# Kernel tuning notes

Hardware: AMD Instinct MI355X
Metric: run time of the kernel (lower is better)

The kernel has to match this reference:

```python
import jax, jax.numpy as jnp
import numpy as np

B, L, S, H, E = 2, 2048, 2048, 16, 64
EPS = 1e-8


def setup_inputs() -> dict:
    key = jax.random.key(0)
    k1, k2, k3, k4, k5 = jax.random.split(key, 5)
    query = jax.random.normal(k1, (B, L, H, E), dtype=jnp.float32)
    key_t = jax.random.normal(k2, (B, S, H, E), dtype=jnp.float32)
    value = jax.random.normal(k3, (B, S, H, E), dtype=jnp.float32)
    mask_miss_k = jax.random.randint(k4, (B, S, 1), 0, 2).astype(bool)
    mask_miss_q = jax.random.randint(k5, (B, L, 1), 0, 2).astype(bool)
    # monotone per-batch positions -> standard causal structure
    pos = jnp.broadcast_to(jnp.arange(L, dtype=jnp.int32)[None, :, None], (B, L, 1))
    return {"query": query, "key": key_t, "value": value,
            "mask_miss_k": mask_miss_k, "mask_miss_q": mask_miss_q,
            "pos": pos, "causal_mask": 1}


def reference(query, key, value, mask_miss_k, mask_miss_q, pos, causal_mask):
    # query: (B,L,H,E); key/value: (B,S,H,E)
    E_ = query.shape[-1]
    scale = 1.0 / np.sqrt(E_)
    scores = jnp.einsum('blhe,bshe->bhls', query, key)  # (B,H,L,S)
    if causal_mask:
        p = pos[..., 0]  # (B,L)
        causal_add = jnp.where(p[:, None, :] > p[:, :, None],
                               -jnp.inf, 0.0).astype(scores.dtype)  # (B,L,S)
        scores = scores + causal_add[:, None, :, :]
    # additive -inf masks for missing keys / queries
    m_k = jnp.where(mask_miss_k[..., 0][:, None, None, :], -jnp.inf, 0.0).astype(scores.dtype)
    m_q = jnp.where(mask_miss_q[..., 0][:, None, :, None], -jnp.inf, 0.0).astype(scores.dtype)
    # NOTE: scale multiplies (scores + M_k) exactly as in the original
    att = jnp.maximum(jax.nn.softmax(scale * (scores + m_k), axis=-1) + m_q, 0.0)
    # entropy of (post-relu, possibly unnormalized) attention weights
    entropy = -jnp.sum(att * jnp.log(jnp.clip(att, EPS, None)), axis=-1)  # (B,H,L)
    entropy = jnp.nan_to_num(entropy, nan=0.0)
    A = jnp.nan_to_num(att)  # dropout p=0 -> identity, then nan_to_num
    V = jnp.einsum('bhls,bshd->blhd', A, value)  # (B,L,H,E)
    return V, A, entropy
```

## Files before the change

kernel.cpp:

```cpp
#include <hip/hip_runtime.h>

#define BB 2
#define LL 2048
#define SS 2048
#define HH 16
#define EE 64
#define HE (HH*EE)
#define BL 128
#define TS 64
#define NT2 32
#define SCALEF 0.125f
#define NEGBIG (-1e30f)

typedef __bf16 bf8 __attribute__((ext_vector_type(8)));
typedef float f4v __attribute__((ext_vector_type(4)));
typedef unsigned int u32;
typedef unsigned short u16;

#define V_ELEMS  ((size_t)BB*LL*HH*EE)
#define A_BASE   (V_ELEMS)
#define ENT_BASE (A_BASE + (size_t)BB*HH*LL*SS)

__device__ __forceinline__ u16 bfb(float f) {
    u32 u = __builtin_bit_cast(u32, f);
    return (u16)((u + 0x7fffu + ((u >> 16) & 1u)) >> 16);
}
__device__ __forceinline__ int swz8(int r) { return (((r) & 7) ^ (((r) >> 3) & 7)) << 4; }

__device__ __forceinline__ f4v mfma16(bf8 a, bf8 b, f4v c) {
    return __builtin_amdgcn_mfma_f32_16x16x32_bf16(a, b, c, 0, 0, 0);
}
__device__ __forceinline__ int maskv(const void* p, int i, int isB) {
    return isB ? (int)((const unsigned char*)p)[i] : ((const int*)p)[i];
}
__device__ __forceinline__ void barrier_lds() {
    asm volatile("s_waitcnt lgkmcnt(0)" ::: "memory");
    __builtin_amdgcn_s_barrier();
    asm volatile("" ::: "memory");
}
__device__ __forceinline__ uint4 pack8(float4 f0, float4 f1) {
    uint4 wv;
    wv.x = bfb(f0.x) | ((u32)bfb(f0.y) << 16);
    wv.y = bfb(f0.z) | ((u32)bfb(f0.w) << 16);
    wv.z = bfb(f1.x) | ((u32)bfb(f1.y) << 16);
    wv.w = bfb(f1.z) | ((u32)bfb(f1.w) << 16);
    return wv;
}

__device__ __forceinline__ void stage128x64(const float* __restrict__ src,
                                            char* lds, int tid) {
    const int r = tid >> 2, seg = tid & 3;
    const float* rp = src + (size_t)r * HE + seg * 16;
    float4 f0 = *(const float4*)(rp + 0);
    float4 f1 = *(const float4*)(rp + 4);
    float4 f2 = *(const float4*)(rp + 8);
    float4 f3 = *(const float4*)(rp + 12);
    const int base = r * 128 + seg * 32;
    *(uint4*)(void*)(lds + ((base +  0) ^ swz8(r))) = pack8(f0, f1);
    *(uint4*)(void*)(lds + ((base + 16) ^ swz8(r))) = pack8(f2, f3);
}

__global__ __launch_bounds__(512) void k_fused(
    const float* __restrict__ Qg, const float* __restrict__ Kg, const float* __restrict__ Vg,
    const void* __restrict__ mk, const void* __restrict__ mq,
    float* __restrict__ outF)
{
    __shared__ __align__(16) char ldsA[16384];
    __shared__ __align__(16) char ldsK[8192];
    __shared__ __align__(16) char ldsVT[8192];
    __shared__ float ldsKM[SS];
    __shared__ int sFlag;

    const int blk = blockIdx.x;
    const int bh  = (blk & 7) + (((blk >> 3) & 3) << 3);
    const int pair = blk >> 5;
    const int b = bh >> 4, h = bh & 15;
    const int tid = threadIdx.x;
    const int w = tid >> 6, lane = tid & 63, g = lane >> 4, le = lane & 15;

    int isB;
    {
        const unsigned char* c = (const unsigned char*)mk;
        unsigned acc = 0;
        #pragma unroll
        for (int j = 0; j < 8; ++j) {
            const int off = tid + j * 512;
            if (off & 3) acc |= c[off];
        }
        if (tid == 0) sFlag = 0;
        __syncthreads();
        if (acc) atomicOr(&sFlag, 1);
        __syncthreads();
        isB = sFlag;
    }
    for (int i = tid; i < SS; i += 512)
        ldsKM[i] = maskv(mk, b * SS + i, isB) ? NEGBIG : 0.f;

    const float* Qb = Qg + (size_t)b * LL * HE + h * EE;
    const float* Kb = Kg + (size_t)b * SS * HE + h * EE;
    const float* Vb = Vg + (size_t)b * SS * HE + h * EE;

    const int kr = tid >> 3, ksg = tid & 7;
    const float* kbase = Kb + (size_t)kr * HE + ksg * 8;
    const int vrp = tid >> 4, vei = tid & 15;
    const float* vbase = Vb + (size_t)(2 * vrp) * HE + vei * 4;

    for (int bi = 0; bi < 2; ++bi) {
        const int band = bi ? (15 - pair) : pair;
        const int l0 = band * BL;
        const int lbase = l0 + w * 16 + g * 4;
        const int ntile = 2 * (band + 1);

        stage128x64(Qb + (size_t)l0 * HE, ldsA, tid);
        __syncthreads();
        const int qr = w * 16 + le;
        bf8 qf0 = *(const bf8*)(void*)(ldsA + ((qr * 128 +  0 + g * 16) ^ swz8(qr)));
        bf8 qf1 = *(const bf8*)(void*)(ldsA + ((qr * 128 + 64 + g * 16) ^ swz8(qr)));
        barrier_lds();

        float M[4], D[4], T[4];
        #pragma unroll
        for (int r = 0; r < 4; ++r) { M[r] = NEGBIG; D[r] = 0.f; T[r] = 0.f; }

        float4 ka = *(const float4*)(kbase);
        float4 kb2 = *(const float4*)(kbase + 4);

        for (int st = 0; st < ntile; ++st) {
            const int s0 = st * TS;
            *(uint4*)(void*)(ldsK + ((kr * 128 + ksg * 16) ^ swz8(kr))) = pack8(ka, kb2);
            if (st + 1 < ntile) {
                const float* kp = kbase + (size_t)((st + 1) * TS) * HE;
                ka = *(const float4*)(kp);
                kb2 = *(const float4*)(kp + 4);
            }
            barrier_lds();

            f4v acc[4];
            float tm[4] = {NEGBIG, NEGBIG, NEGBIG, NEGBIG};
            #pragma unroll
            for (int cb = 0; cb < 4; ++cb) {
                const int sr = cb * 16 + le;
                bf8 k0 = *(const bf8*)(void*)(ldsK + ((sr * 128 +  0 + g * 16) ^ swz8(sr)));
                bf8 k1 = *(const bf8*)(void*)(ldsK + ((sr * 128 + 64 + g * 16) ^ swz8(sr)));
                f4v a = {0.f, 0.f, 0.f, 0.f};
                a = mfma16(qf0, k0, a);
                a = mfma16(qf1, k1, a);
                const float km = ldsKM[s0 + cb * 16 + le];
                const int s = s0 + cb * 16 + le;
                #pragma unroll
                for (int r = 0; r < 4; ++r) {
                    float z = a[r] * SCALEF + km;
                    if (s > lbase + r) z = NEGBIG;
                    acc[cb][r] = z;
                    tm[r] = fmaxf(tm[r], z);
                }
            }
            #pragma unroll
            for (int r = 0; r < 4; ++r) {
                #pragma unroll
                for (int msk = 1; msk < 16; msk <<= 1)
                    tm[r] = fmaxf(tm[r], __shfl_xor(tm[r], msk));
                const float mn  = fmaxf(M[r], tm[r]);
                const float fre = __expf(M[r] - mn);
                float ed = 0.f, et = 0.f;
                #pragma unroll
                for (int cb = 0; cb < 4; ++cb) {
                    const float z = acc[cb][r];
                    const float e = __expf(z - mn);
                    ed += e; et += e * z;
                }
                D[r] = D[r] * fre + ed;
                T[r] = T[r] * fre + et;
                M[r] = mn;
            }
            barrier_lds();
        }

        float C[4];
        #pragma unroll
        for (int r = 0; r < 4; ++r) {
            #pragma unroll
            for (int msk = 1; msk < 16; msk <<= 1) {
                const float Mo = __shfl_xor(M[r], msk);
                const float Do = __shfl_xor(D[r], msk);
                const float To = __shfl_xor(T[r], msk);
                const float mn = fmaxf(M[r], Mo);
                const float fa = __expf(M[r] - mn);
                const float fb = __expf(Mo  - mn);
                D[r] = D[r] * fa + Do * fb;
                T[r] = T[r] * fa + To * fb;
                M[r] = mn;
            }
            const int l = lbase + r;
            const bool valid = (M[r] > -1e29f) && (maskv(mq, b * LL + l, isB) == 0);
            C[r] = valid ? (M[r] + __logf(D[r])) : 1e30f;
            const float ent = valid ? (C[r] - T[r] / D[r]) : 0.f;
            if (le == 0) outF[ENT_BASE + (size_t)bh * LL + l] = ent;
        }

        f4v O[4];
        #pragma unroll
        for (int eb = 0; eb < 4; ++eb) O[eb] = (f4v){0.f, 0.f, 0.f, 0.f};

        ka  = *(const float4*)(kbase);
        kb2 = *(const float4*)(kbase + 4);
        float4 va  = *(const float4*)(vbase);
        float4 vb2 = *(const float4*)(vbase + HE);

        for (int st = 0; st < ntile; ++st) {
            const int s0 = st * TS;
            *(uint4*)(void*)(ldsK + ((kr * 128 + ksg * 16) ^ swz8(kr))) = pack8(ka, kb2);
            {
                const float* pa_ = &va.x;
                const float* pb_ = &vb2.x;
                #pragma unroll
                for (int i = 0; i < 4; ++i) {
                    const int e = vei * 4 + i;
                    const u32 pk = (u32)bfb(pa_[i]) | ((u32)bfb(pb_[i]) << 16);
                    *(u32*)(void*)(ldsVT + ((e * 128 + vrp * 4) ^ swz8(e))) = pk;
                }
            }
            if (st + 1 < ntile) {
                const float* kp = kbase + (size_t)((st + 1) * TS) * HE;
                const float* vp = vbase + (size_t)((st + 1) * TS) * HE;
                ka  = *(const float4*)(kp);
                kb2 = *(const float4*)(kp + 4);
                va  = *(const float4*)(vp);
                vb2 = *(const float4*)(vp + HE);
            }
            barrier_lds();

            f4v acc[4];
            #pragma unroll
            for (int cb = 0; cb < 4; ++cb) {
                const int sr = cb * 16 + le;
                bf8 k0 = *(const bf8*)(void*)(ldsK + ((sr * 128 +  0 + g * 16) ^ swz8(sr)));
                bf8 k1 = *(const bf8*)(void*)(ldsK + ((sr * 128 + 64 + g * 16) ^ swz8(sr)));
                f4v a = {0.f, 0.f, 0.f, 0.f};
                a = mfma16(qf0, k0, a);
                a = mfma16(qf1, k1, a);
                acc[cb] = a;
            }
            #pragma unroll
            for (int cb = 0; cb < 4; ++cb) {
                const float km = ldsKM[s0 + cb * 16 + le];
                const int s = s0 + cb * 16 + le;
                #pragma unroll
                for (int r = 0; r < 4; ++r) {
                    float z = acc[cb][r] * SCALEF + km;
                    if (s > lbase + r) z = NEGBIG;
                    const float p = __expf(z - C[r]);
                    const int row = w * 16 + g * 4 + r;
                    *(u16*)(void*)(ldsA + ((row * 128 + (cb * 16 + le) * 2) ^ swz8(row))) = bfb(p);
                    outF[A_BASE + ((size_t)bh * LL + (l0 + row)) * SS + s] = p;
                }
            }
            barrier_lds();

            const int prow = w * 16 + le;
            #pragma unroll
            for (int kkb = 0; kkb < 2; ++kkb) {
                bf8 pa = *(const bf8*)(void*)(ldsA + ((prow * 128 + kkb * 64 + g * 16) ^ swz8(prow)));
                #pragma unroll
                for (int eb = 0; eb < 4; ++eb) {
                    const int e = eb * 16 + le;
                    bf8 vb = *(const bf8*)(void*)(ldsVT + ((e * 128 + kkb * 64 + g * 16) ^ swz8(e)));
                    O[eb] = mfma16(pa, vb, O[eb]);
                }
            }
            barrier_lds();
        }

        {
            const int r = tid >> 2, cseg = tid & 3;
            const float4 zz = {0.f, 0.f, 0.f, 0.f};
            for (int st = ntile; st < NT2; ++st) {
                float* dst = &outF[A_BASE + ((size_t)bh * LL + (l0 + r)) * SS + st * TS + cseg * 16];
                #pragma unroll
                for (int i = 0; i < 4; ++i) *(float4*)(dst + i * 4) = zz;
            }
        }

        #pragma unroll
        for (int eb = 0; eb < 4; ++eb) {
            #pragma unroll
            for (int r = 0; r < 4; ++r) {
                const int l = lbase + r;
                outF[((size_t)(b * LL + l) * HH + h) * EE + eb * 16 + le] = O[eb][r];
            }
        }
        __syncthreads();
    }
}

extern "C" void kernel_launch(void* const* d_in, const int* in_sizes, int n_in,
                              void* d_out, int out_size, void* d_ws, size_t ws_size,
                              hipStream_t stream) {
    const float* Q = (const float*)d_in[0];
    const float* K = (const float*)d_in[1];
    const float* V = (const float*)d_in[2];
    const void* mk = d_in[3];
    const void* mq = d_in[4];
    float* outF = (float*)d_out;

    dim3 blk(512), grid(BB * HH * 8);
    hipLaunchKernelGGL(k_fused, grid, blk, 0, stream, Q, K, V, mk, mq, outF);
}
```

Measured before the change: 236.7 us.

## Double-buffer K/V LDS tiles, skip fully-masked wave tiles, use nontemporal stores

Measured after the change: 569.6 us. +140.7%, slower.

```diff
diff --git a/kernel.cpp b/kernel.cpp
--- a/kernel.cpp
+++ b/kernel.cpp
@@ -46,6 +46,8 @@
     wv.w = bfb(f1.z) | ((u32)bfb(f1.w) << 16);
     return wv;
 }
+__device__ __forceinline__ void st_nt(float v, float* p) { __builtin_nontemporal_store(v, p); }
+__device__ __forceinline__ void st_nt4(f4v v, float* p) { __builtin_nontemporal_store(v, (f4v*)p); }
 
 __device__ __forceinline__ void stage128x64(const float* __restrict__ src,
                                             char* lds, int tid) {
@@ -65,9 +67,9 @@
     const void* __restrict__ mk, const void* __restrict__ mq,
     float* __restrict__ outF)
 {
-    __shared__ __align__(16) char ldsA[16384];
-    __shared__ __align__(16) char ldsK[8192];
-    __shared__ __align__(16) char ldsVT[8192];
+    __shared__ __align__(16) char ldsP[16384];
+    __shared__ __align__(16) char ldsK[2][8192];
+    __shared__ __align__(16) char ldsVT[2][8192];
     __shared__ float ldsKM[SS];
     __shared__ int sFlag;
 
@@ -102,6 +104,7 @@
 
     const int kr = tid >> 3, ksg = tid & 7;
     const float* kbase = Kb + (size_t)kr * HE + ksg * 8;
+    const int koff = (kr * 128 + ksg * 16) ^ swz8(kr);
     const int vrp = tid >> 4, vei = tid & 15;
     const float* vbase = Vb + (size_t)(2 * vrp) * HE + vei * 4;
 
@@ -109,13 +112,14 @@
         const int band = bi ? (15 - pair) : pair;
         const int l0 = band * BL;
         const int lbase = l0 + w * 16 + g * 4;
+        const int whi = l0 + w * 16 + 15;
         const int ntile = 2 * (band + 1);
 
-        stage128x64(Qb + (size_t)l0 * HE, ldsA, tid);
+        stage128x64(Qb + (size_t)l0 * HE, ldsP, tid);
         __syncthreads();
         const int qr = w * 16 + le;
-        bf8 qf0 = *(const bf8*)(void*)(ldsA + ((qr * 128 +  0 + g * 16) ^ swz8(qr)));
-        bf8 qf1 = *(const bf8*)(void*)(ldsA + ((qr * 128 + 64 + g * 16) ^ swz8(qr)));
+        bf8 qf0 = *(const bf8*)(void*)(ldsP + ((qr * 128 +  0 + g * 16) ^ swz8(qr)));
+        bf8 qf1 = *(const bf8*)(void*)(ldsP + ((qr * 128 + 64 + g * 16) ^ swz8(qr)));
         barrier_lds();
 
         float M[4], D[4], T[4];
@@ -124,56 +128,65 @@
 
         float4 ka = *(const float4*)(kbase);
         float4 kb2 = *(const float4*)(kbase + 4);
+        *(uint4*)(void*)(&ldsK[0][0] + koff) = pack8(ka, kb2);
+        if (ntile > 1) {
+            const float* kp = kbase + (size_t)TS * HE;
+            ka = *(const float4*)(kp); kb2 = *(const float4*)(kp + 4);
+        }
+        barrier_lds();
+        int cur = 0;
 
         for (int st = 0; st < ntile; ++st) {
             const int s0 = st * TS;
-            *(uint4*)(void*)(ldsK + ((kr * 128 + ksg * 16) ^ swz8(kr))) = pack8(ka, kb2);
             if (st + 1 < ntile) {
-                const float* kp = kbase + (size_t)((st + 1) * TS) * HE;
-                ka = *(const float4*)(kp);
-                kb2 = *(const float4*)(kp + 4);
+                *(uint4*)(void*)(&ldsK[cur ^ 1][0] + koff) = pack8(ka, kb2);
+                if (st + 2 < ntile) {
+                    const float* kp = kbase + (size_t)(st + 2) * TS * HE;
+                    ka = *(const float4*)(kp); kb2 = *(const float4*)(kp + 4);
+                }
+            }
+            if (s0 <= whi) {
+                f4v acc[4];
+                float tm[4] = {NEGBIG, NEGBIG, NEGBIG, NEGBIG};
+                #pragma unroll
+                for (int cb = 0; cb < 4; ++cb) {
+                    const int sr = cb * 16 + le;
+                    bf8 k0 = *(const bf8*)(void*)(&ldsK[cur][0] + ((sr * 128 +  0 + g * 16) ^ swz8(sr)));
+                    bf8 k1 = *(const bf8*)(void*)(&ldsK[cur][0] + ((sr * 128 + 64 + g * 16) ^ swz8(sr)));
+                    f4v a = {0.f, 0.f, 0.f, 0.f};
+                    a = mfma16(qf0, k0, a);
+                    a = mfma16(qf1, k1, a);
+                    const float km = ldsKM[s0 + cb * 16 + le];
+                    const int s = s0 + cb * 16 + le;
+                    #pragma unroll
+                    for (int r = 0; r < 4; ++r) {
+                        float z = a[r] * SCALEF + km;
+                        if (s > lbase + r) z = NEGBIG;
+                        acc[cb][r] = z;
+                        tm[r] = fmaxf(tm[r], z);
+                    }
+                }
+                #pragma unroll
+                for (int r = 0; r < 4; ++r) {
+                    #pragma unroll
+                    for (int msk = 1; msk < 16; msk <<= 1)
+                        tm[r] = fmaxf(tm[r], __shfl_xor(tm[r], msk));
+                    const float mn  = fmaxf(M[r], tm[r]);
+                    const float fre = __expf(M[r] - mn);
+                    float ed = 0.f, et = 0.f;
+                    #pragma unroll
+                    for (int cb = 0; cb < 4; ++cb) {
+                        const float z = acc[cb][r];
+                        const float e = __expf(z - mn);
+                        ed += e; et += e * z;
+                    }
+                    D[r] = D[r] * fre + ed;
+                    T[r] = T[r] * fre + et;
+                    M[r] = mn;
+                }
             }
             barrier_lds();
-
-            f4v acc[4];
-            float tm[4] = {NEGBIG, NEGBIG, NEGBIG, NEGBIG};
-            #pragma unroll
-            for (int cb = 0; cb < 4; ++cb) {
-                const int sr = cb * 16 + le;
-                bf8 k0 = *(const bf8*)(void*)(ldsK + ((sr * 128 +  0 + g * 16) ^ swz8(sr)));
-                bf8 k1 = *(const bf8*)(void*)(ldsK + ((sr * 128 + 64 + g * 16) ^ swz8(sr)));
-                f4v a = {0.f, 0.f, 0.f, 0.f};
-                a = mfma16(qf0, k0, a);
-                a = mfma16(qf1, k1, a);
-                const float km = ldsKM[s0 + cb * 16 + le];
-                const int s = s0 + cb * 16 + le;
-                #pragma unroll
-                for (int r = 0; r < 4; ++r) {
-                    float z = a[r] * SCALEF + km;
-                    if (s > lbase + r) z = NEGBIG;
-                    acc[cb][r] = z;
-                    tm[r] = fmaxf(tm[r], z);
-                }
-            }
-            #pragma unroll
-            for (int r = 0; r < 4; ++r) {
-                #pragma unroll
-                for (int msk = 1; msk < 16; msk <<= 1)
-                    tm[r] = fmaxf(tm[r], __shfl_xor(tm[r], msk));
-                const float mn  = fmaxf(M[r], tm[r]);
-                const float fre = __expf(M[r] - mn);
-                float ed = 0.f, et = 0.f;
-                #pragma unroll
-                for (int cb = 0; cb < 4; ++cb) {
-                    const float z = acc[cb][r];
-                    const float e = __expf(z - mn);
-                    ed += e; et += e * z;
-                }
-                D[r] = D[r] * fre + ed;
-                T[r] = T[r] * fre + et;
-                M[r] = mn;
-            }
-            barrier_lds();
+            cur ^= 1;
         }
 
         float C[4];
@@ -195,7 +208,7 @@
             const bool valid = (M[r] > -1e29f) && (maskv(mq, b * LL + l, isB) == 0);
             C[r] = valid ? (M[r] + __logf(D[r])) : 1e30f;
             const float ent = valid ? (C[r] - T[r] / D[r]) : 0.f;
-            if (le == 0) outF[ENT_BASE + (size_t)bh * LL + l] = ent;
+            if (le == 0) st_nt(ent, &outF[ENT_BASE + (size_t)bh * LL + l]);
         }
 
         f4v O[4];
@@ -206,78 +219,110 @@
         kb2 = *(const float4*)(kbase + 4);
         float4 va  = *(const float4*)(vbase);
         float4 vb2 = *(const float4*)(vbase + HE);
+        *(uint4*)(void*)(&ldsK[0][0] + koff) = pack8(ka, kb2);
+        {
+            const float* pa_ = &va.x; const float* pb_ = &vb2.x;
+            #pragma unroll
+            for (int i = 0; i < 4; ++i) {
+                const int e = vei * 4 + i;
+                const u32 pk = (u32)bfb(pa_[i]) | ((u32)bfb(pb_[i]) << 16);
+                *(u32*)(void*)(&ldsVT[0][0] + ((e * 128 + vrp * 4) ^ swz8(e))) = pk;
+            }
+        }
+        if (ntile > 1) {
+            const float* kp = kbase + (size_t)TS * HE;
+            const float* vp = vbase + (size_t)TS * HE;
+            ka = *(const float4*)(kp); kb2 = *(const float4*)(kp + 4);
+            va = *(const float4*)(vp); vb2 = *(const float4*)(vp + HE);
+        }
+        barrier_lds();
+        cur = 0;
+        float* const Arow0 = outF + A_BASE + ((size_t)bh * LL + l0) * SS;
 
         for (int st = 0; st < ntile; ++st) {
             const int s0 = st * TS;
-            *(uint4*)(void*)(ldsK + ((kr * 128 + ksg * 16) ^ swz8(kr))) = pack8(ka, kb2);
-            {
-                const float* pa_ = &va.x;
-                const float* pb_ = &vb2.x;
-                #pragma unroll
-                for (int i = 0; i < 4; ++i) {
-                    const int e = vei * 4 + i;
-                    const u32 pk = (u32)bfb(pa_[i]) | ((u32)bfb(pb_[i]) << 16);
-                    *(u32*)(void*)(ldsVT + ((e * 128 + vrp * 4) ^ swz8(e))) = pk;
-                }
-            }
             if (st + 1 < ntile) {
-                const float* kp = kbase + (size_t)((st + 1) * TS) * HE;
-                const float* vp = vbase + (size_t)((st + 1) * TS) * HE;
-                ka  = *(const float4*)(kp);
-                kb2 = *(const float4*)(kp + 4);
-                va  = *(const float4*)(vp);
-                vb2 = *(const float4*)(vp + HE);
+                *(uint4*)(void*)(&ldsK[cur ^ 1][0] + koff) = pack8(ka, kb2);
+                {
+                    const float* pa_ = &va.x; const float* pb_ = &vb2.x;
+                    #pragma unroll
+                    for (int i = 0; i < 4; ++i) {
+                        const int e = vei * 4 + i;
+                        const u32 pk = (u32)bfb(pa_[i]) | ((u32)bfb(pb_[i]) << 16);
+                        *(u32*)(void*)(&ldsVT[cur ^ 1][0] + ((e * 128 + vrp * 4) ^ swz8(e))) = pk;
+                    }
+                }
+                if (st + 2 < ntile) {
+                    const float* kp = kbase + (size_t)(st + 2) * TS * HE;
+                    const float* vp = vbase + (size_t)(st + 2) * TS * HE;
+                    ka = *(const float4*)(kp); kb2 = *(const float4*)(kp + 4);
+                    va = *(const float4*)(vp); vb2 = *(const float4*)(vp + HE);
+                }
+            }
+            const bool active = (s0 <= whi);
+            if (active) {
+                f4v acc[4];
+                #pragma unroll
+                for (int cb = 0; cb < 4; ++cb) {
+                    const int sr = cb * 16 + le;
+                    bf8 k0 = *(const bf8*)(void*)(&ldsK[cur][0] + ((sr * 128 +  0 + g * 16) ^ swz8(sr)));
+                    bf8 k1 = *(const bf8*)(void*)(&ldsK[cur][0] + ((sr * 128 + 64 + g * 16) ^ swz8(sr)));
+                    f4v a = {0.f, 0.f, 0.f, 0.f};
+                    a = mfma16(qf0, k0, a);
+                    a = mfma16(qf1, k1, a);
+                    acc[cb] = a;
+                }
+                #pragma unroll
+                for (int cb = 0; cb < 4; ++cb) {
+                    const float km = ldsKM[s0 + cb * 16 + le];
+                    const int s = s0 + cb * 16 + le;
+                    #pragma unroll
+                    for (int r = 0; r < 4; ++r) {
+                        float z = acc[cb][r] * SCALEF + km;
+                        if (s > lbase + r) z = NEGBIG;
+                        const float p = __expf(z - C[r]);
+                        const int row = w * 16 + g * 4 + r;
+                        *(u16*)(void*)(ldsP + ((row * 128 + (cb * 16 + le) * 2) ^ swz8(row))) = bfb(p);
+                        st_nt(p, Arow0 + (size_t)row * SS + s);
+                    }
+                }
+            } else {
+                #pragma unroll
+                for (int cb = 0; cb < 4; ++cb) {
+                    const int s = s0 + cb * 16 + le;
+                    #pragma unroll
+                    for (int r = 0; r < 4; ++r) {
+                        const int row = w * 16 + g * 4 + r;
+                        st_nt(0.f, Arow0 + (size_t)row * SS + s);
+                    }
+                }
             }
             barrier_lds();
 
-            f4v acc[4];
-            #pragma unroll
-            for (int cb = 0; cb < 4; ++cb) {
-                const int sr = cb * 16 + le;
-                bf8 k0 = *(const bf8*)(void*)(ldsK + ((sr * 128 +  0 + g * 16) ^ swz8(sr)));
-                bf8 k1 = *(const bf8*)(void*)(ldsK + ((sr * 128 + 64 + g * 16) ^ swz8(sr)));
-                f4v a = {0.f, 0.f, 0.f, 0.f};
-                a = mfma16(qf0, k0, a);
-                a = mfma16(qf1, k1, a);
-                acc[cb] = a;
-            }
-            #pragma unroll
-            for (int cb = 0; cb < 4; ++cb) {
-                const float km = ldsKM[s0 + cb * 16 + le];
-                const int s = s0 + cb * 16 + le;
-                #pragma unroll
-                for (int r = 0; r < 4; ++r) {
-                    float z = acc[cb][r] * SCALEF + km;
-                    if (s > lbase + r) z = NEGBIG;
-                    const float p = __expf(z - C[r]);
-                    const int row = w * 16 + g * 4 + r;
-                    *(u16*)(void*)(ldsA + ((row * 128 + (cb * 16 + le) * 2) ^ swz8(row))) = bfb(p);
-                    outF[A_BASE + ((size_t)bh * LL + (l0 + row)) * SS + s] = p;
+            if (active) {
+                const int prow = w * 16 + le;
+                #pragma unroll
+                for (int kkb = 0; kkb < 2; ++kkb) {
+                    bf8 pa = *(const bf8*)(void*)(ldsP + ((prow * 128 + kkb * 64 + g * 16) ^ swz8(prow)));
+                    #pragma unroll
+                    for (int eb = 0; eb < 4; ++eb) {
+                        const int e = eb * 16 + le;
+                        bf8 vb = *(const bf8*)(void*)(&ldsVT[cur][0] + ((e * 128 + kkb * 64 + g * 16) ^ swz8(e)));
+                        O[eb] = mfma16(pa, vb, O[eb]);
+                    }
                 }
             }
             barrier_lds();
-
-            const int prow = w * 16 + le;
-            #pragma unroll
-            for (int kkb = 0; kkb < 2; ++kkb) {
-                bf8 pa = *(const bf8*)(void*)(ldsA + ((prow * 128 + kkb * 64 + g * 16) ^ swz8(prow)));
-                #pragma unroll
-                for (int eb = 0; eb < 4; ++eb) {
-                    const int e = eb * 16 + le;
-                    bf8 vb = *(const bf8*)(void*)(ldsVT + ((e * 128 + kkb * 64 + g * 16) ^ swz8(e)));
-                    O[eb] = mfma16(pa, vb, O[eb]);
-                }
-            }
-            barrier_lds();
+            cur ^= 1;
         }
 
         {
             const int r = tid >> 2, cseg = tid & 3;
-            const float4 zz = {0.f, 0.f, 0.f, 0.f};
+            const f4v zz = {0.f, 0.f, 0.f, 0.f};
             for (int st = ntile; st < NT2; ++st) {
-                float* dst = &outF[A_BASE + ((size_t)bh * LL + (l0 + r)) * SS + st * TS + cseg * 16];
-                #pragma unroll
-                for (int i = 0; i < 4; ++i) *(float4*)(dst + i * 4) = zz;
+                float* dst = Arow0 + (size_t)r * SS + st * TS + cseg * 16;
+                #pragma unroll
+                for (int i = 0; i < 4; ++i) st_nt4(zz, dst + i * 4);
             }
         }
 
@@ -286,7 +331,7 @@
             #pragma unroll
             for (int r = 0; r < 4; ++r) {
                 const int l = lbase + r;
-                outF[((size_t)(b * LL + l) * HH + h) * EE + eb * 16 + le] = O[eb][r];
+                st_nt(O[eb][r], &outF[((size_t)(b * LL + l) * HH + h) * EE + eb * 16 + le]);
             }
         }
         __syncthreads();
```

## Load Q/K fragments directly from global, per-wave causal skip, double-buffer V

Applied to the files above, without the earlier changes.

After: 358.2 us. 51.3% more time.

```diff
diff --git a/kernel.cpp b/kernel.cpp
--- a/kernel.cpp
+++ b/kernel.cpp
@@ -46,18 +46,11 @@
     wv.w = bfb(f1.z) | ((u32)bfb(f1.w) << 16);
     return wv;
 }
-
-__device__ __forceinline__ void stage128x64(const float* __restrict__ src,
-                                            char* lds, int tid) {
-    const int r = tid >> 2, seg = tid & 3;
-    const float* rp = src + (size_t)r * HE + seg * 16;
-    float4 f0 = *(const float4*)(rp + 0);
-    float4 f1 = *(const float4*)(rp + 4);
-    float4 f2 = *(const float4*)(rp + 8);
-    float4 f3 = *(const float4*)(rp + 12);
-    const int base = r * 128 + seg * 32;
-    *(uint4*)(void*)(lds + ((base +  0) ^ swz8(r))) = pack8(f0, f1);
-    *(uint4*)(void*)(lds + ((base + 16) ^ swz8(r))) = pack8(f2, f3);
+__device__ __forceinline__ bf8 frag8(const float* p) {
+    float4 f0 = *(const float4*)(p);
+    float4 f1 = *(const float4*)(p + 4);
+    uint4 u = pack8(f0, f1);
+    return __builtin_bit_cast(bf8, u);
 }
 
 __global__ __launch_bounds__(512) void k_fused(
@@ -65,9 +58,8 @@
     const void* __restrict__ mk, const void* __restrict__ mq,
     float* __restrict__ outF)
 {
-    __shared__ __align__(16) char ldsA[16384];
-    __shared__ __align__(16) char ldsK[8192];
-    __shared__ __align__(16) char ldsVT[8192];
+    __shared__ __align__(16) char ldsP[16384];
+    __shared__ __align__(16) char ldsVT[2][8192];
     __shared__ float ldsKM[SS];
     __shared__ int sFlag;
 
@@ -95,53 +87,42 @@
     }
     for (int i = tid; i < SS; i += 512)
         ldsKM[i] = maskv(mk, b * SS + i, isB) ? NEGBIG : 0.f;
+    __syncthreads();
 
     const float* Qb = Qg + (size_t)b * LL * HE + h * EE;
     const float* Kb = Kg + (size_t)b * SS * HE + h * EE;
     const float* Vb = Vg + (size_t)b * SS * HE + h * EE;
 
-    const int kr = tid >> 3, ksg = tid & 7;
-    const float* kbase = Kb + (size_t)kr * HE + ksg * 8;
     const int vrp = tid >> 4, vei = tid & 15;
     const float* vbase = Vb + (size_t)(2 * vrp) * HE + vei * 4;
+    char* const myP = ldsP + w * 2048;
+    const float* krow0 = Kb + (size_t)le * HE + g * 8;
 
     for (int bi = 0; bi < 2; ++bi) {
         const int band = bi ? (15 - pair) : pair;
         const int l0 = band * BL;
         const int lbase = l0 + w * 16 + g * 4;
+        const int ta = (l0 + w * 16 + 15) >> 6;
         const int ntile = 2 * (band + 1);
 
-        stage128x64(Qb + (size_t)l0 * HE, ldsA, tid);
-        __syncthreads();
-        const int qr = w * 16 + le;
-        bf8 qf0 = *(const bf8*)(void*)(ldsA + ((qr * 128 +  0 + g * 16) ^ swz8(qr)));
-        bf8 qf1 = *(const bf8*)(void*)(ldsA + ((qr * 128 + 64 + g * 16) ^ swz8(qr)));
-        barrier_lds();
+        const float* qrow = Qb + (size_t)(l0 + w * 16 + le) * HE + g * 8;
+        bf8 qf0 = frag8(qrow);
+        bf8 qf1 = frag8(qrow + 32);
 
         float M[4], D[4], T[4];
         #pragma unroll
         for (int r = 0; r < 4; ++r) { M[r] = NEGBIG; D[r] = 0.f; T[r] = 0.f; }
 
-        float4 ka = *(const float4*)(kbase);
-        float4 kb2 = *(const float4*)(kbase + 4);
-
-        for (int st = 0; st < ntile; ++st) {
+        for (int st = 0; st <= ta; ++st) {
             const int s0 = st * TS;
-            *(uint4*)(void*)(ldsK + ((kr * 128 + ksg * 16) ^ swz8(kr))) = pack8(ka, kb2);
-            if (st + 1 < ntile) {
-                const float* kp = kbase + (size_t)((st + 1) * TS) * HE;
-                ka = *(const float4*)(kp);
-                kb2 = *(const float4*)(kp + 4);
-            }
-            barrier_lds();
-
+            const float* kt = krow0 + (size_t)s0 * HE;
             f4v acc[4];
             float tm[4] = {NEGBIG, NEGBIG, NEGBIG, NEGBIG};
             #pragma unroll
             for (int cb = 0; cb < 4; ++cb) {
-                const int sr = cb * 16 + le;
-                bf8 k0 = *(const bf8*)(void*)(ldsK + ((sr * 128 +  0 + g * 16) ^ swz8(sr)));
-                bf8 k1 = *(const bf8*)(void*)(ldsK + ((sr * 128 + 64 + g * 16) ^ swz8(sr)));
+                const float* kp = kt + (size_t)(cb * 16) * HE;
+                bf8 k0 = frag8(kp);
+                bf8 k1 = frag8(kp + 32);
                 f4v a = {0.f, 0.f, 0.f, 0.f};
                 a = mfma16(qf0, k0, a);
                 a = mfma16(qf1, k1, a);
@@ -173,7 +154,6 @@
                 T[r] = T[r] * fre + et;
                 M[r] = mn;
             }
-            barrier_lds();
         }
 
         float C[4];
@@ -198,87 +178,95 @@
             if (le == 0) outF[ENT_BASE + (size_t)bh * LL + l] = ent;
         }
 
+        float* const Arow0 = outF + A_BASE + ((size_t)bh * LL + l0) * SS;
+
+        {
+            const int rr = lane >> 2, cc = lane & 3;
+            float* dst0 = Arow0 + (size_t)(w * 16 + rr) * SS;
+            const f4v zz = {0.f, 0.f, 0.f, 0.f};
+            for (int c = (ta + 1) * TS + cc * 4; c < SS; c += 16)
+                *(f4v*)(void*)(dst0 + c) = zz;
+        }
+
         f4v O[4];
         #pragma unroll
         for (int eb = 0; eb < 4; ++eb) O[eb] = (f4v){0.f, 0.f, 0.f, 0.f};
 
-        ka  = *(const float4*)(kbase);
-        kb2 = *(const float4*)(kbase + 4);
         float4 va  = *(const float4*)(vbase);
         float4 vb2 = *(const float4*)(vbase + HE);
+        {
+            const float* pa_ = &va.x; const float* pb_ = &vb2.x;
+            #pragma unroll
+            for (int i = 0; i < 4; ++i) {
+                const int e = vei * 4 + i;
+                const u32 pk = (u32)bfb(pa_[i]) | ((u32)bfb(pb_[i]) << 16);
+                *(u32*)(void*)(&ldsVT[0][0] + ((e * 128 + vrp * 4) ^ swz8(e))) = pk;
+            }
+        }
+        if (ntile > 1) {
+            const float* vp = vbase + (size_t)TS * HE;
+            va = *(const float4*)(vp); vb2 = *(const float4*)(vp + HE);
+        }
+        barrier_lds();
+        int cur = 0;
 
         for (int st = 0; st < ntile; ++st) {
             const int s0 = st * TS;
-            *(uint4*)(void*)(ldsK + ((kr * 128 + ksg * 16) ^ swz8(kr))) = pack8(ka, kb2);
-            {
-                const float* pa_ = &va.x;
-                const float* pb_ = &vb2.x;
+            if (st + 1 < ntile) {
+                const float* pa_ = &va.x; const float* pb_ = &vb2.x;
                 #pragma unroll
                 for (int i = 0; i < 4; ++i) {
                     const int e = vei * 4 + i;
                     const u32 pk = (u32)bfb(pa_[i]) | ((u32)bfb(pb_[i]) << 16);
-                    *(u32*)(void*)(ldsVT + ((e * 128 + vrp * 4) ^ swz8(e))) = pk;
-                }
-            }
-            if (st + 1 < ntile) {
-                const float* kp = kbase + (size_t)((st + 1) * TS) * HE;
-                const float* vp = vbase + (size_t)((st + 1) * TS) * HE;
-                ka  = *(const float4*)(kp);
-                kb2 = *(const float4*)(kp + 4);
-                va  = *(const float4*)(vp);
-                vb2 = *(const float4*)(vp + HE);
+                    *(u32*)(void*)(&ldsVT[cur ^ 1][0] + ((e * 128 + vrp * 4) ^ swz8(e))) = pk;
+                }
+                if (st + 2 < ntile) {
+                    const float* vp = vbase + (size_t)(st + 2) * TS * HE;
+                    va = *(const float4*)(vp); vb2 = *(const float4*)(vp + HE);
+                }
+            }
+            if (st <= ta) {
+                const float* kt = krow0 + (size_t)s0 * HE;
+                f4v acc[4];
+                #pragma unroll
+                for (int cb = 0; cb < 4; ++cb) {
+                    const float* kp = kt + (size_t)(cb * 16) * HE;
+                    bf8 k0 = frag8(kp);
+                    bf8 k1 = frag8(kp + 32);
+                    f4v a = {0.f, 0.f, 0.f, 0.f};
+                    a = mfma16(qf0, k0, a);
+                    a = mfma16(qf1, k1, a);
+                    acc[cb] = a;
+                }
+                #pragma unroll
+                for (int cb = 0; cb < 4; ++cb) {
+                    const float km = ldsKM[s0 + cb * 16 + le];
+                    const int s = s0 + cb * 16 + le;
+                    #pragma unroll
+                    for (int r = 0; r < 4; ++r) {
+                        float z = acc[cb][r] * SCALEF + km;
+                        if (s > lbase + r) z = NEGBIG;
+                        const float p = __expf(z - C[r]);
+                        const int row = g * 4 + r;
+                        *(u16*)(void*)(myP + ((row * 128 + (cb * 16 + le) * 2) ^ swz8(row))) = bfb(p);
+                        outF[A_BASE + ((size_t)bh * LL + (l0 + w * 16 + row)) * SS + s] = p;
+                    }
+                }
+                asm volatile("s_waitcnt lgkmcnt(0)" ::: "memory");
+
+                #pragma unroll
+                for (int kkb = 0; kkb < 2; ++kkb) {
+                    bf8 pa = *(const bf8*)(void*)(myP + ((le * 128 + kkb * 64 + g * 16) ^ swz8(le)));
+                    #pragma unroll
+                    for (int eb = 0; eb < 4; ++eb) {
+                        const int e = eb * 16 + le;
+                        bf8 vb = *(const bf8*)(void*)(&ldsVT[cur][0] + ((e * 128 + kkb * 64 + g * 16) ^ swz8(e)));
+                        O[eb] = mfma16(pa, vb, O[eb]);
+                    }
+                }
             }
             barrier_lds();
-
-            f4v acc[4];
-            #pragma unroll
-            for (int cb = 0; cb < 4; ++cb) {
-                const int sr = cb * 16 + le;
-                bf8 k0 = *(const bf8*)(void*)(ldsK + ((sr * 128 +  0 + g * 16) ^ swz8(sr)));
-                bf8 k1 = *(const bf8*)(void*)(ldsK + ((sr * 128 + 64 + g * 16) ^ swz8(sr)));
-                f4v a = {0.f, 0.f, 0.f, 0.f};
-                a = mfma16(qf0, k0, a);
-                a = mfma16(qf1, k1, a);
-                acc[cb] = a;
-            }
-            #pragma unroll
-            for (int cb = 0; cb < 4; ++cb) {
-                const float km = ldsKM[s0 + cb * 16 + le];
-                const int s = s0 + cb * 16 + le;
-                #pragma unroll
-                for (int r = 0; r < 4; ++r) {
-                    float z = acc[cb][r] * SCALEF + km;
-                    if (s > lbase + r) z = NEGBIG;
-                    const float p = __expf(z - C[r]);
-                    const int row = w * 16 + g * 4 + r;
-                    *(u16*)(void*)(ldsA + ((row * 128 + (cb * 16 + le) * 2) ^ swz8(row))) = bfb(p);
-                    outF[A_BASE + ((size_t)bh * LL + (l0 + row)) * SS + s] = p;
-                }
-            }
-            barrier_lds();
-
-            const int prow = w * 16 + le;
-            #pragma unroll
-            for (int kkb = 0; kkb < 2; ++kkb) {
-                bf8 pa = *(const bf8*)(void*)(ldsA + ((prow * 128 + kkb * 64 + g * 16) ^ swz8(prow)));
-                #pragma unroll
-                for (int eb = 0; eb < 4; ++eb) {
-                    const int e = eb * 16 + le;
-                    bf8 vb = *(const bf8*)(void*)(ldsVT + ((e * 128 + kkb * 64 + g * 16) ^ swz8(e)));
-                    O[eb] = mfma16(pa, vb, O[eb]);
-                }
-            }
-            barrier_lds();
-        }
-
-        {
-            const int r = tid >> 2, cseg = tid & 3;
-            const float4 zz = {0.f, 0.f, 0.f, 0.f};
-            for (int st = ntile; st < NT2; ++st) {
-                float* dst = &outF[A_BASE + ((size_t)bh * LL + (l0 + r)) * SS + st * TS + cseg * 16];
-                #pragma unroll
-                for (int i = 0; i < 4; ++i) *(float4*)(dst + i * 4) = zz;
-            }
+            cur ^= 1;
         }
 
         #pragma unroll
```
